# Optimization experiments

Hardware: AMD Instinct MI355X
Metric: run time of the kernel (lower is better)

## Reference

```python
import jax, jax.numpy as jnp
import numpy as np
import math

B, S, C = 4, 8, 1024
DK = 1024
MAX_LEN = 8192
TOKEN_IND = 4095


def setup_inputs() -> dict:
    key = jax.random.key(0)
    k1, k2, k3, k4 = jax.random.split(key, 4)
    x = jax.random.normal(k1, (B, S, C), dtype=jnp.float32)
    W = jax.random.normal(k2, (C, 3 * DK), dtype=jnp.float32) * (1.0 / math.sqrt(C))
    b = jnp.zeros((3 * DK,), dtype=jnp.float32)
    key_cache = jax.random.normal(k3, (B, MAX_LEN, DK), dtype=jnp.float32)
    value_cache = jax.random.normal(k4, (B, MAX_LEN, DK), dtype=jnp.float32)
    return {"x": x, "W": W, "b": b, "key_cache": key_cache,
            "value_cache": value_cache, "token_ind": TOKEN_IND}


def reference(x, W, b, key_cache, value_cache, token_ind):
    # decode step: only the last token of x is used
    x_last = x[:, -1:, :]                        # [B, 1, C]
    qkv = x_last @ W + b                         # [B, 1, 3*dk]
    q, k_new, v_new = jnp.split(qkv, 3, axis=-1)  # each [B, 1, dk]
    dk = q.shape[-1]

    # scatter new k/v into cache at token_ind, then slice valid prefix
    key_cache = key_cache.at[:, token_ind:token_ind + 1, :].set(k_new)
    value_cache = value_cache.at[:, token_ind:token_ind + 1, :].set(v_new)
    size = token_ind + 1
    k = key_cache[:, :size, :]                   # [B, size, dk]
    v = value_cache[:, :size, :]                 # [B, size, dk]

    # scores for the single query against the whole valid cache
    weights = jnp.einsum('btc,bTc->btT', q, k) / math.sqrt(dk)  # [B, 1, size]

    # faithful broadcast quirk of the original: tril mask (size,size)
    # broadcasts weights [B,1,size] up to [B,size,size]
    mask = jnp.tril(jnp.ones((size, size), dtype=weights.dtype))
    logits = jnp.where(mask == 0, jnp.asarray(-9e15, weights.dtype), weights)  # [B, size, size]
    attention = jax.nn.softmax(logits, axis=-1)
    values = jnp.einsum('btT,bTc->btc', attention, v)  # [B, size, dk]
    return values
```

## Files before the change

### kernel.cpp

```cpp
#include <hip/hip_runtime.h>
#include <stdint.h>

#define B_      4
#define S_      8
#define C_      1024
#define DK_     1024
#define MAXLEN_ 8192
#define SIZE_   4096
#define NCH     64
#define CHR     64
#define NTOK    (SIZE_ - 1)

typedef unsigned short ushort_t;
typedef unsigned int   uint_t;
typedef float f32x4 __attribute__((ext_vector_type(4)));

__device__ __forceinline__ float bf2f(ushort_t u) {
    union { uint_t u; float f; } v; v.u = ((uint_t)u) << 16; return v.f;
}
__device__ __forceinline__ ushort_t f2bf(float f) {
    union { float f; uint_t u; } v; v.f = f;
    uint_t u = v.u;
    uint_t lsb = (u >> 16) & 1u;
    u += 0x7fffu + lsb;
    return (ushort_t)(u >> 16);
}

__global__ void __launch_bounds__(256) k_qkv_partial(
        const float* __restrict__ x, const float* __restrict__ W,
        float* __restrict__ part) {
    __shared__ float xs[B_][128];
    __shared__ float red[8][32][16];
    int t  = threadIdx.x;
    int cg_ = t & 31;
    int rg  = t >> 5;
    int c0 = blockIdx.x * 128;
    int r0 = blockIdx.y * 128;

    for (int i = t; i < B_ * 128; i += 256) {
        int b = i >> 7, r = i & 127;
        xs[b][r] = x[((b * S_) + (S_ - 1)) * C_ + r0 + r];
    }
    __syncthreads();

    float acc[B_][4] = {};
    const float* wp = W + (size_t)(r0 + rg * 16) * (3 * DK_) + c0 + cg_ * 4;
#pragma unroll 8
    for (int i = 0; i < 16; ++i) {
        f32x4 wv = *(const f32x4*)(wp + (size_t)i * (3 * DK_));
        int r = rg * 16 + i;
#pragma unroll
        for (int b = 0; b < B_; ++b) {
            float xv = xs[b][r];
            acc[b][0] += xv * wv[0];
            acc[b][1] += xv * wv[1];
            acc[b][2] += xv * wv[2];
            acc[b][3] += xv * wv[3];
        }
    }
#pragma unroll
    for (int b = 0; b < B_; ++b)
#pragma unroll
        for (int cc = 0; cc < 4; ++cc)
            red[rg][cg_][b * 4 + cc] = acc[b][cc];
    __syncthreads();

    if (t < 32) {
#pragma unroll
        for (int b = 0; b < B_; ++b) {
            float s0 = 0.f, s1 = 0.f, s2 = 0.f, s3 = 0.f;
#pragma unroll
            for (int r = 0; r < 8; ++r) {
                s0 += red[r][t][b * 4 + 0];
                s1 += red[r][t][b * 4 + 1];
                s2 += red[r][t][b * 4 + 2];
                s3 += red[r][t][b * 4 + 3];
            }
            f32x4 v = { s0, s1, s2, s3 };
            *(f32x4*)(part + (size_t)blockIdx.y * (B_ * 3 * DK_) + b * (3 * DK_) + c0 + t * 4) = v;
        }
    }
}

__global__ void __launch_bounds__(256) k_qkv_finish(
        const float* __restrict__ part, const float* __restrict__ bias,
        float* __restrict__ qkvws) {
    int i   = blockIdx.x * 256 + threadIdx.x;
    int bq  = i / 3072;
    int col = i - bq * 3072;
    float s = bias[col];
#pragma unroll
    for (int rt = 0; rt < 8; ++rt) s += part[rt * (B_ * 3 * DK_) + i];
    qkvws[(col >> 10) * (B_ * DK_) + bq * DK_ + (col & (DK_ - 1))] = s;
}

__global__ void __launch_bounds__(1024) k_scores_sum(
        const float* __restrict__ kc, const float* __restrict__ vc,
        const float* __restrict__ qkvws, ushort_t* __restrict__ es_bf,
        float* __restrict__ Ec, ushort_t* __restrict__ Pc) {
    __shared__ float es_l[CHR];
    __shared__ float ec_l[16];
    int t    = threadIdx.x;
    int c    = blockIdx.x;
    int b    = blockIdx.y;
    int lane = t & 63;
    int wv   = t >> 6;

    {
        const float* qp = qkvws + b * DK_ + lane * 4;
        f32x4 q0 = *(const f32x4*)(qp);
        f32x4 q1 = *(const f32x4*)(qp + 256);
        f32x4 q2 = *(const f32x4*)(qp + 512);
        f32x4 q3 = *(const f32x4*)(qp + 768);
        int j0 = c * CHR + wv * 4;
        float esum = 0.f;
#pragma unroll
        for (int r = 0; r < 4; ++r) {
            int j = j0 + r;
            const float* kp = (j == NTOK)
                ? (qkvws + (B_ * DK_) + b * DK_)
                : (kc + ((size_t)b * MAXLEN_ + j) * DK_);
            kp += lane * 4;
            f32x4 k0 = *(const f32x4*)(kp);
            f32x4 k1 = *(const f32x4*)(kp + 256);
            f32x4 k2 = *(const f32x4*)(kp + 512);
            f32x4 k3 = *(const f32x4*)(kp + 768);
            float acc = k0[0]*q0[0] + k0[1]*q0[1] + k0[2]*q0[2] + k0[3]*q0[3]
                      + k1[0]*q1[0] + k1[1]*q1[1] + k1[2]*q1[2] + k1[3]*q1[3]
                      + k2[0]*q2[0] + k2[1]*q2[1] + k2[2]*q2[2] + k2[3]*q2[3]
                      + k3[0]*q3[0] + k3[1]*q3[1] + k3[2]*q3[2] + k3[3]*q3[3];
#pragma unroll
            for (int off = 32; off > 0; off >>= 1) acc += __shfl_down(acc, off, 64);
            if (lane == 0) {
                float e = __expf(acc * 0.03125f);
                es_l[wv * 4 + r] = e;
                es_bf[b * SIZE_ + j] = f2bf(e);
                esum += e;
            }
        }
        if (lane == 0) ec_l[wv] = esum;
    }
    __syncthreads();
    if (t == 0) {
        float s = 0.f;
#pragma unroll
        for (int i = 0; i < 16; ++i) s += ec_l[i];
        Ec[b * NCH + c] = s;
    }

    {
        const float* vbase = vc + ((size_t)b * MAXLEN_ + c * CHR) * DK_ + t;
        float a = 0.f;
        bool last = (c == NCH - 1);
#pragma unroll 8
        for (int r = 0; r < CHR - 1; ++r)
            a += es_l[r] * vbase[(size_t)r * DK_];
        {
            float u = last ? qkvws[2 * (B_ * DK_) + b * DK_ + t]
                           : vbase[(size_t)(CHR - 1) * DK_];
            a += es_l[CHR - 1] * u;
        }
        Pc[((size_t)(b * NCH + c)) * DK_ + t] = f2bf(a);
    }
}

__global__ void __launch_bounds__(1024) k_out(
        const float* __restrict__ vc, const float* __restrict__ qkvws,
        const ushort_t* __restrict__ es_bf, const float* __restrict__ Ec,
        const ushort_t* __restrict__ Pc, float* __restrict__ out) {
    __shared__ float es_l[CHR];
    __shared__ float invS[CHR];
    int t = threadIdx.x;
    int c = blockIdx.x;
    int b = blockIdx.y;

    if (t < 64) {
        float e = bf2f(es_bf[b * SIZE_ + c * CHR + t]);
        es_l[t] = e;
        float p = (t < c) ? Ec[b * NCH + t] : 0.f;
#pragma unroll
        for (int off = 32; off > 0; off >>= 1) p += __shfl_down(p, off, 64);
        float E0 = __shfl(p, 0, 64);
        float sc = e;
#pragma unroll
        for (int off = 1; off < 64; off <<= 1) {
            float o = __shfl_up(sc, off, 64);
            if (t >= off) sc += o;
        }
        invS[t] = 1.0f / (E0 + sc);
    }
    __syncthreads();

    float a = 0.f;
    {
        const ushort_t* pp = Pc + (size_t)b * NCH * DK_ + t;
        for (int cc = 0; cc < c; ++cc) a += bf2f(pp[(size_t)cc * DK_]);
    }

    const float* vbase = vc + ((size_t)b * MAXLEN_ + c * CHR) * DK_ + t;
    float* obase = out + ((size_t)b * SIZE_ + c * CHR) * DK_ + t;
    bool last = (c == NCH - 1);
#pragma unroll 8
    for (int r = 0; r < CHR - 1; ++r) {
        a += es_l[r] * vbase[(size_t)r * DK_];
        __builtin_nontemporal_store(a * invS[r], obase + (size_t)r * DK_);
    }
    {
        float u = last ? qkvws[2 * (B_ * DK_) + b * DK_ + t]
                       : vbase[(size_t)(CHR - 1) * DK_];
        a += es_l[CHR - 1] * u;
        __builtin_nontemporal_store(a * invS[CHR - 1], obase + (size_t)(CHR - 1) * DK_);
    }
}

extern "C" void kernel_launch(void* const* d_in, const int* in_sizes, int n_in,
                              void* d_out, int out_size, void* d_ws, size_t ws_size,
                              hipStream_t stream) {
    (void)in_sizes; (void)n_in; (void)out_size; (void)ws_size;
    const float* x    = (const float*)d_in[0];
    const float* W    = (const float*)d_in[1];
    const float* bias = (const float*)d_in[2];
    const float* kc   = (const float*)d_in[3];
    const float* vc   = (const float*)d_in[4];
    float* out        = (float*)d_out;

    float* ws       = (float*)d_ws;
    float* part     = ws;
    float* qkvws    = ws + 131072;
    ushort_t* es_bf = (ushort_t*)(ws + 143360);
    float* Ec       = ws + 151552;
    ushort_t* Pc    = (ushort_t*)ws;

    hipLaunchKernelGGL(k_qkv_partial, dim3(24, 8), dim3(256),  0, stream, x, W, part);
    hipLaunchKernelGGL(k_qkv_finish,  dim3(48),    dim3(256),  0, stream, part, bias, qkvws);
    hipLaunchKernelGGL(k_scores_sum,  dim3(64, 4), dim3(1024), 0, stream, kc, vc, qkvws, es_bf, Ec, Pc);
    hipLaunchKernelGGL(k_out,         dim3(64, 4), dim3(1024), 0, stream, vc, qkvws, es_bf, Ec, Pc, out);
}
```

Before: 304.3 us.

## Split chunk rows across thread groups with vectorized V loads in scan kernels

Both the chunk-sum and output kernels now assign each group of 256 threads a quarter of the chunk's 64 rows, with each thread handling 4 columns through float4 loads. Before, every thread walked all 64 rows serially for one scalar column. Partial sums are combined through shared memory, and in the output kernel each group gets an exclusive prefix over earlier groups. The prefix over earlier chunks' partial sums is also split across the four groups. This shortens the serial dependency chain and widens memory accesses, at the cost of extra shared memory, more barriers, and 16 float4 registers per thread.

```diff
diff --git a/kernel.cpp b/kernel.cpp
--- a/kernel.cpp
+++ b/kernel.cpp
@@ -100,11 +100,15 @@
         float* __restrict__ Ec, ushort_t* __restrict__ Pc) {
     __shared__ float es_l[CHR];
     __shared__ float ec_l[16];
+    __shared__ f32x4 sub[4][256];
     int t    = threadIdx.x;
     int c    = blockIdx.x;
     int b    = blockIdx.y;
     int lane = t & 63;
     int wv   = t >> 6;
+    int rg   = t >> 8;
+    int tc   = t & 255;
+    int d0   = tc * 4;
 
     {
         const float* qp = qkvws + b * DK_ + lane * 4;
@@ -149,18 +153,26 @@
     }
 
     {
-        const float* vbase = vc + ((size_t)b * MAXLEN_ + c * CHR) * DK_ + t;
-        float a = 0.f;
-        bool last = (c == NCH - 1);
-#pragma unroll 8
-        for (int r = 0; r < CHR - 1; ++r)
-            a += es_l[r] * vbase[(size_t)r * DK_];
-        {
-            float u = last ? qkvws[2 * (B_ * DK_) + b * DK_ + t]
-                           : vbase[(size_t)(CHR - 1) * DK_];
-            a += es_l[CHR - 1] * u;
-        }
-        Pc[((size_t)(b * NCH + c)) * DK_ + t] = f2bf(a);
+        const float* vbase = vc + ((size_t)b * MAXLEN_ + c * CHR + rg * 16) * DK_ + d0;
+        bool subst = (c == NCH - 1) && (rg == 3);
+        f32x4 a = { 0.f, 0.f, 0.f, 0.f };
+#pragma unroll
+        for (int i = 0; i < 16; ++i) {
+            const float* vp = (subst && i == 15)
+                ? (qkvws + 2 * (B_ * DK_) + b * DK_ + d0)
+                : (vbase + (size_t)i * DK_);
+            f32x4 u = *(const f32x4*)(vp);
+            a += es_l[rg * 16 + i] * u;
+        }
+        sub[rg][tc] = a;
+        __syncthreads();
+        if (rg == 0) {
+            f32x4 tot = a + sub[1][tc] + sub[2][tc] + sub[3][tc];
+            ushort4 pv;
+            pv.x = f2bf(tot[0]); pv.y = f2bf(tot[1]);
+            pv.z = f2bf(tot[2]); pv.w = f2bf(tot[3]);
+            *(ushort4*)(Pc + ((size_t)(b * NCH + c)) * DK_ + d0) = pv;
+        }
     }
 }
 
@@ -170,9 +182,14 @@
         const ushort_t* __restrict__ Pc, float* __restrict__ out) {
     __shared__ float es_l[CHR];
     __shared__ float invS[CHR];
-    int t = threadIdx.x;
-    int c = blockIdx.x;
-    int b = blockIdx.y;
+    __shared__ f32x4 sub[4][256];
+    __shared__ f32x4 pre[4][256];
+    int t  = threadIdx.x;
+    int c  = blockIdx.x;
+    int b  = blockIdx.y;
+    int rg = t >> 8;
+    int tc = t & 255;
+    int d0 = tc * 4;
 
     if (t < 64) {
         float e = bf2f(es_bf[b * SIZE_ + c * CHR + t]);
@@ -189,27 +206,50 @@
         }
         invS[t] = 1.0f / (E0 + sc);
     }
-    __syncthreads();
-
-    float a = 0.f;
-    {
-        const ushort_t* pp = Pc + (size_t)b * NCH * DK_ + t;
-        for (int cc = 0; cc < c; ++cc) a += bf2f(pp[(size_t)cc * DK_]);
-    }
-
-    const float* vbase = vc + ((size_t)b * MAXLEN_ + c * CHR) * DK_ + t;
-    float* obase = out + ((size_t)b * SIZE_ + c * CHR) * DK_ + t;
-    bool last = (c == NCH - 1);
-#pragma unroll 8
-    for (int r = 0; r < CHR - 1; ++r) {
-        a += es_l[r] * vbase[(size_t)r * DK_];
-        __builtin_nontemporal_store(a * invS[r], obase + (size_t)r * DK_);
-    }
-    {
-        float u = last ? qkvws[2 * (B_ * DK_) + b * DK_ + t]
-                       : vbase[(size_t)(CHR - 1) * DK_];
-        a += es_l[CHR - 1] * u;
-        __builtin_nontemporal_store(a * invS[CHR - 1], obase + (size_t)(CHR - 1) * DK_);
+
+    f32x4 vrow[16];
+    {
+        const float* vbase = vc + ((size_t)b * MAXLEN_ + c * CHR + rg * 16) * DK_ + d0;
+        bool subst = (c == NCH - 1) && (rg == 3);
+#pragma unroll
+        for (int i = 0; i < 16; ++i) {
+            const float* vp = (subst && i == 15)
+                ? (qkvws + 2 * (B_ * DK_) + b * DK_ + d0)
+                : (vbase + (size_t)i * DK_);
+            vrow[i] = *(const f32x4*)(vp);
+        }
+    }
+
+    {
+        f32x4 p = { 0.f, 0.f, 0.f, 0.f };
+        const ushort_t* pp = Pc + (size_t)b * NCH * DK_ + d0;
+        for (int cc = rg; cc < c; cc += 4) {
+            ushort4 pv = *(const ushort4*)(pp + (size_t)cc * DK_);
+            p[0] += bf2f(pv.x); p[1] += bf2f(pv.y);
+            p[2] += bf2f(pv.z); p[3] += bf2f(pv.w);
+        }
+        pre[rg][tc] = p;
+    }
+    __syncthreads();
+
+    f32x4 a = { 0.f, 0.f, 0.f, 0.f };
+#pragma unroll
+    for (int i = 0; i < 16; ++i) a += es_l[rg * 16 + i] * vrow[i];
+    sub[rg][tc] = a;
+    __syncthreads();
+
+    f32x4 acc = pre[0][tc] + pre[1][tc] + pre[2][tc] + pre[3][tc];
+#pragma unroll
+    for (int g = 0; g < 3; ++g)
+        if (g < rg) acc += sub[g][tc];
+
+    float* obase = out + ((size_t)b * SIZE_ + c * CHR + rg * 16) * DK_ + d0;
+#pragma unroll
+    for (int i = 0; i < 16; ++i) {
+        acc += es_l[rg * 16 + i] * vrow[i];
+        float is = invS[rg * 16 + i];
+        f32x4 ov = { acc[0] * is, acc[1] * is, acc[2] * is, acc[3] * is };
+        __builtin_nontemporal_store(ov, (f32x4*)(obase + (size_t)i * DK_));
     }
 }
 
```

New measurement: 294.6 us. 3.2% less time.
